# Kernel tuning notes

Measured on AMD Instinct MI355X. Metric: run time of the kernel, lower is better.

The kernel has to match this reference:

```python
import jax, jax.numpy as jnp
import numpy as np

MARGIN = 0.0


def setup_inputs() -> dict:
    key = jax.random.key(0)
    k1, k2, k3 = jax.random.split(key, 3)
    n, d = 8192, 128
    inputs = jax.random.normal(k1, (n, d), dtype=jnp.float32)
    targets = jax.random.randint(k2, (n,), 0, 512, dtype=jnp.int64)
    cids = jax.random.randint(k3, (n,), 0, 8, dtype=jnp.int64)
    return {"inputs": inputs, "targets": targets, "cids": cids}


def _margin_ranking_loss(x1, x2, margin):
    # nn.MarginRankingLoss with y=1: mean(max(0, -(x1 - x2) + margin))
    return jnp.mean(jnp.maximum(x2 - x1 + margin, 0.0))


def reference(inputs, targets, cids):
    n = inputs.shape[0]
    # pairwise euclidean distance matrix [n, n]
    sq = jnp.sum(inputs * inputs, axis=1)              # [n]
    d2 = sq[:, None] + sq[None, :] - 2.0 * (inputs @ inputs.T)
    dist = jnp.sqrt(jnp.clip(d2, 1e-12, 1e12))         # [n, n]

    mask = targets[:, None] == targets[None, :]        # [n, n] same-identity
    # view_mask (cids) is computed in the original but never used

    # hardest positive (max over same-id, incl. self) and hardest negative (min over diff-id)
    pos_masked = jnp.where(mask, dist, -jnp.inf)
    neg_masked = jnp.where(mask, jnp.inf, dist)
    dist_ap = jnp.max(pos_masked, axis=1)              # [n]
    dist_an = jnp.min(neg_masked, axis=1)              # [n]
    p2_ind = jnp.argmax(pos_masked, axis=1)            # [n]
    n1_ind = jnp.argmin(neg_masked, axis=1)            # [n]

    # secondary neighbors: hardest-negative of the hardest negative,
    # hardest-positive of the hardest positive (row lookups)
    dist_n12 = dist_an[n1_ind]                         # min of dist[n1_ind] over ~mask[n1_ind]
    dist_p12 = dist_ap[p2_ind]                         # max of dist[p2_ind] over mask[p2_ind]

    loss = (_margin_ranking_loss(dist_an, dist_ap, MARGIN)
            + 0.1 * _margin_ranking_loss(dist_n12, dist_ap, MARGIN)
            + 0.1 * _margin_ranking_loss(dist_an, dist_p12, MARGIN))
    prec = jnp.mean((dist_an > dist_ap).astype(jnp.float32))
    return loss, prec, dist
```

## Files before the change

kernel.cpp:

```cpp
#include <hip/hip_runtime.h>

#define NROWS 8192
#define DDIM 128

typedef unsigned short u16;
typedef unsigned int u32;
typedef unsigned long long u64;
typedef __attribute__((ext_vector_type(4))) float f32x4;
typedef __attribute__((ext_vector_type(4), aligned(8))) float f32x4u;
typedef __attribute__((ext_vector_type(2))) float f32x2;
typedef __attribute__((ext_vector_type(4))) int i32x4;
typedef __attribute__((ext_vector_type(8))) short short8;

__device__ __forceinline__ u16 f32_to_bf16(float f){
  u32 u = __float_as_uint(f);
  u32 r = (u + 0x7FFFu + ((u >> 16) & 1u)) >> 16;
  return (u16)r;
}
__device__ __forceinline__ float bf16_to_f32(u16 h){ return __uint_as_float(((u32)h) << 16); }

__global__ __launch_bounds__(256) void pack_kernel(const float* __restrict__ in,
                                                   u16* __restrict__ phi, u16* __restrict__ plo,
                                                   float* __restrict__ sq,
                                                   u64* __restrict__ pos_key, u64* __restrict__ neg_key){
  int t = blockIdx.x * 256 + threadIdx.x;
  if (t < NROWS){ pos_key[t] = 0ull; neg_key[t] = 0xFFFFFFFFFFFFFFFFull; }
  int r = t >> 4, s = t & 15;
  const float* src = in + (size_t)r * DDIM + s * 8;
  f32x4 a = *(const f32x4*)(src);
  f32x4 b = *(const f32x4*)(src + 4);
  float x[8] = {a.x, a.y, a.z, a.w, b.x, b.y, b.z, b.w};
  short8 hv, lv;
  float ss = 0.f;
  #pragma unroll
  for (int j = 0; j < 8; ++j){
    u16 h = f32_to_bf16(x[j]);
    u16 l = f32_to_bf16(x[j] - bf16_to_f32(h));
    hv[j] = (short)h; lv[j] = (short)l;
    ss += x[j] * x[j];
  }
  size_t dst = (((size_t)(r >> 4) * 4 + (s >> 2)) * 64 + (s & 3) * 16 + (r & 15)) * 8;
  *(short8*)(phi + dst) = hv;
  *(short8*)(plo + dst) = lv;
  #pragma unroll
  for (int m = 1; m < 16; m <<= 1) ss += __shfl_xor(ss, m, 64);
  if (s == 0) sq[r] = ss;
}

__global__ __launch_bounds__(256, 2) void dist_kernel(
    const u16* __restrict__ phi, const u16* __restrict__ plo,
    const float* __restrict__ sq, const int* __restrict__ tgt,
    float* __restrict__ dist, u64* __restrict__ pos_key, u64* __restrict__ neg_key)
{
  int id = blockIdx.x;
  int xcd = id & 7, r9 = id >> 3;
  int cx = xcd >> 1, cy = xcd & 1;
  const int bi = cx * 16 + (r9 >> 5);
  const int bj = cy * 32 + (r9 & 31);

  const int tid = threadIdx.x;
  const int w = tid >> 6, lane = tid & 63;
  const int wr = w >> 1, wc = w & 1;
  const int lr = lane & 15, g = lane >> 4;

  f32x4 acc[4][4] = {};

  short8 bufA[2][8], bufB[2][8];
  #pragma unroll
  for (int m = 0; m < 4; ++m){
    size_t offA = ((size_t)(((bi * 8 + wr * 4 + m) * 4 + 0) * 64) + lane) * 8;
    bufA[0][m * 2 + 0] = *(const short8*)(phi + offA);
    bufA[0][m * 2 + 1] = *(const short8*)(plo + offA);
    size_t offB = ((size_t)(((bj * 8 + wc * 4 + m) * 4 + 0) * 64) + lane) * 8;
    bufB[0][m * 2 + 0] = *(const short8*)(phi + offB);
    bufB[0][m * 2 + 1] = *(const short8*)(plo + offB);
  }
  #pragma unroll
  for (int kk = 0; kk < 4; ++kk){
    const int cur = kk & 1, nxt = cur ^ 1;
    if (kk < 3){
      #pragma unroll
      for (int m = 0; m < 4; ++m){
        size_t offA = ((size_t)(((bi * 8 + wr * 4 + m) * 4 + (kk + 1)) * 64) + lane) * 8;
        bufA[nxt][m * 2 + 0] = *(const short8*)(phi + offA);
        bufA[nxt][m * 2 + 1] = *(const short8*)(plo + offA);
        size_t offB = ((size_t)(((bj * 8 + wc * 4 + m) * 4 + (kk + 1)) * 64) + lane) * 8;
        bufB[nxt][m * 2 + 0] = *(const short8*)(phi + offB);
        bufB[nxt][m * 2 + 1] = *(const short8*)(plo + offB);
      }
    }
    #pragma unroll
    for (int m = 0; m < 4; ++m)
      #pragma unroll
      for (int n = 0; n < 4; ++n){
        acc[m][n] = __builtin_amdgcn_mfma_f32_16x16x32_bf16(bufB[cur][n*2+0], bufA[cur][m*2+0], acc[m][n], 0, 0, 0);
        acc[m][n] = __builtin_amdgcn_mfma_f32_16x16x32_bf16(bufB[cur][n*2+1], bufA[cur][m*2+0], acc[m][n], 0, 0, 0);
        acc[m][n] = __builtin_amdgcn_mfma_f32_16x16x32_bf16(bufB[cur][n*2+0], bufA[cur][m*2+1], acc[m][n], 0, 0, 0);
      }
  }

  f32x4 sqc[4]; i32x4 tcv[4]; int cbase[4];
  #pragma unroll
  for (int n = 0; n < 4; ++n){
    cbase[n] = bj * 128 + wc * 64 + n * 16 + g * 4;
    sqc[n] = *(const f32x4*)(sq + cbase[n]);
    tcv[n] = *(const i32x4*)(tgt + cbase[n]);
  }
  #pragma unroll
  for (int m = 0; m < 4; ++m){
    const int grow = bi * 128 + wr * 64 + m * 16 + lr;
    const float sqr = sq[grow];
    const int tr = tgt[grow];
    float bpv = -1.f, bnv = 3.0e38f; int bpc = 0x7FFFFFFF, bnc = 0x7FFFFFFF;
    float* drow = dist + (size_t)grow * NROWS;
    #pragma unroll
    for (int n = 0; n < 4; ++n){
      f32x4 dd4;
      #pragma unroll
      for (int r = 0; r < 4; ++r){
        float d2 = sqr + sqc[n][r] - 2.f * acc[m][n][r];
        d2 = fminf(fmaxf(d2, 1e-12f), 1e12f);
        dd4[r] = __builtin_amdgcn_sqrtf(d2);
        if (tr == tcv[n][r]){
          if (d2 > bpv){ bpv = d2; bpc = cbase[n] + r; }
        } else {
          if (d2 < bnv){ bnv = d2; bnc = cbase[n] + r; }
        }
      }
      *(f32x4u*)(drow + cbase[n]) = dd4;
    }
    #pragma unroll
    for (int msk = 16; msk <= 32; msk <<= 1){
      float ov = __shfl_xor(bpv, msk, 64); int oc = __shfl_xor(bpc, msk, 64);
      if (ov > bpv || (ov == bpv && oc < bpc)){ bpv = ov; bpc = oc; }
      ov = __shfl_xor(bnv, msk, 64); oc = __shfl_xor(bnc, msk, 64);
      if (ov < bnv || (ov == bnv && oc < bnc)){ bnv = ov; bnc = oc; }
    }
    if (g == 0){
      if (bpv >= 0.f)
        atomicMax(&pos_key[grow],
                  ((u64)__float_as_uint(__builtin_amdgcn_sqrtf(bpv)) << 32) | (u64)(0xFFFFFFFFu - (u32)bpc));
      if (bnv < 3.0e38f)
        atomicMin(&neg_key[grow],
                  ((u64)__float_as_uint(__builtin_amdgcn_sqrtf(bnv)) << 32) | (u64)(u32)bnc);
    }
  }
}

__global__ __launch_bounds__(1024) void final_kernel(const u64* __restrict__ pk, const u64* __restrict__ nk,
                                                     float* __restrict__ out){
  __shared__ float s_ap[NROWS];
  __shared__ float s_an[NROWS];
  int tid = threadIdx.x;
  int p2r[8], n1r[8];
  #pragma unroll
  for (int j = 0; j < 8; ++j){
    int i = tid + j * 1024;
    u64 p = pk[i], q = nk[i];
    s_ap[i] = __uint_as_float((u32)(p >> 32));
    s_an[i] = __uint_as_float((u32)(q >> 32));
    p2r[j] = (int)(0xFFFFFFFFu - (u32)(p & 0xFFFFFFFFu));
    n1r[j] = (int)(u32)(q & 0xFFFFFFFFu);
  }
  __syncthreads();
  float s1 = 0.f, s2 = 0.f, s3 = 0.f; float pc = 0.f;
  #pragma unroll
  for (int j = 0; j < 8; ++j){
    int i = tid + j * 1024;
    float a = s_ap[i], b = s_an[i];
    float n12 = s_an[n1r[j]];
    float p12 = s_ap[p2r[j]];
    s1 += fmaxf(a - b, 0.f);
    s2 += fmaxf(a - n12, 0.f);
    s3 += fmaxf(p12 - b, 0.f);
    pc += (b > a) ? 1.f : 0.f;
  }
  __syncthreads();
  float* r1 = s_ap; float* r2 = s_ap + 1024; float* r3 = s_an; float* r4 = s_an + 1024;
  r1[tid] = s1; r2[tid] = s2; r3[tid] = s3; r4[tid] = pc;
  __syncthreads();
  for (int s = 512; s > 0; s >>= 1){
    if (tid < s){ r1[tid] += r1[tid + s]; r2[tid] += r2[tid + s]; r3[tid] += r3[tid + s]; r4[tid] += r4[tid + s]; }
    __syncthreads();
  }
  if (tid == 0){
    float inv = 1.f / (float)NROWS;
    out[0] = r1[0] * inv + 0.1f * (r2[0] * inv) + 0.1f * (r3[0] * inv);
    out[1] = r4[0] * inv;
  }
}

extern "C" void kernel_launch(void* const* d_in, const int* in_sizes, int n_in,
                              void* d_out, int out_size, void* d_ws, size_t ws_size,
                              hipStream_t stream){
  const float* inputs = (const float*)d_in[0];
  const int* targets = (const int*)d_in[1];
  float* out = (float*)d_out;
  char* ws = (char*)d_ws;

  u16* phi = (u16*)ws;
  u16* plo = (u16*)(ws + (2u << 20));
  float* sq = (float*)(ws + (4u << 20));
  u64* pos_key = (u64*)(ws + (4u << 20) + (64u << 10));
  u64* neg_key = (u64*)(ws + (4u << 20) + (128u << 10));

  pack_kernel<<<(NROWS * 16) / 256, 256, 0, stream>>>(inputs, phi, plo, sq, pos_key, neg_key);
  dist_kernel<<<64 * 64, 256, 0, stream>>>(phi, plo, sq, targets, out + 2, pos_key, neg_key);
  final_kernel<<<1, 1024, 0, stream>>>(pos_key, neg_key, out);
}
```

Before: 128.1 us.

## Make dist blocks persistent over four column tiles with cross-tile prefetch

Each block now handles four consecutive 128x128 column tiles of one row block, so the grid shrinks from 4096 to 1024 blocks. The next tile's first K-slice is prefetched during the last MFMA step of the current tile, which hides load latency across tiles and cuts block launch overhead. The trade-off is less parallel slack per CU and possible extra register pressure. The epilogue stores and atomics stay serial per tile, so there is less chance to overlap them with compute from other blocks.

```diff
diff --git a/kernel.cpp b/kernel.cpp
--- a/kernel.cpp
+++ b/kernel.cpp
@@ -53,98 +53,102 @@
     float* __restrict__ dist, u64* __restrict__ pos_key, u64* __restrict__ neg_key)
 {
   int id = blockIdx.x;
-  int xcd = id & 7, r9 = id >> 3;
-  int cx = xcd >> 1, cy = xcd & 1;
-  const int bi = cx * 16 + (r9 >> 5);
-  const int bj = cy * 32 + (r9 & 31);
+  int xcd = id & 7, r7 = id >> 3;
+  const int bi = (xcd >> 1) * 16 + (r7 >> 3);
+  const int strip = (xcd & 1) * 8 + (r7 & 7);
+  const int bj0 = strip * 4;
 
   const int tid = threadIdx.x;
   const int w = tid >> 6, lane = tid & 63;
   const int wr = w >> 1, wc = w & 1;
   const int lr = lane & 15, g = lane >> 4;
 
-  f32x4 acc[4][4] = {};
-
   short8 bufA[2][8], bufB[2][8];
-  #pragma unroll
-  for (int m = 0; m < 4; ++m){
-    size_t offA = ((size_t)(((bi * 8 + wr * 4 + m) * 4 + 0) * 64) + lane) * 8;
-    bufA[0][m * 2 + 0] = *(const short8*)(phi + offA);
-    bufA[0][m * 2 + 1] = *(const short8*)(plo + offA);
-    size_t offB = ((size_t)(((bj * 8 + wc * 4 + m) * 4 + 0) * 64) + lane) * 8;
-    bufB[0][m * 2 + 0] = *(const short8*)(phi + offB);
-    bufB[0][m * 2 + 1] = *(const short8*)(plo + offB);
-  }
-  #pragma unroll
-  for (int kk = 0; kk < 4; ++kk){
-    const int cur = kk & 1, nxt = cur ^ 1;
-    if (kk < 3){
+
+  #define LOADS(p, BJ, KK)                                                              \
+    _Pragma("unroll")                                                                   \
+    for (int m_ = 0; m_ < 4; ++m_){                                                     \
+      size_t offA = ((size_t)(((bi * 8 + wr * 4 + m_) * 4 + (KK)) * 64) + lane) * 8;    \
+      bufA[p][m_ * 2 + 0] = *(const short8*)(phi + offA);                               \
+      bufA[p][m_ * 2 + 1] = *(const short8*)(plo + offA);                               \
+      size_t offB = ((size_t)((((BJ) * 8 + wc * 4 + m_) * 4 + (KK)) * 64) + lane) * 8;  \
+      bufB[p][m_ * 2 + 0] = *(const short8*)(phi + offB);                               \
+      bufB[p][m_ * 2 + 1] = *(const short8*)(plo + offB);                               \
+    }
+
+  LOADS(0, bj0, 0);
+
+  for (int t = 0; t < 4; ++t){
+    const int bj = bj0 + t;
+
+    f32x4 acc[4][4] = {};
+
+    #pragma unroll
+    for (int kk = 0; kk < 4; ++kk){
+      const int cur = kk & 1, nxt = cur ^ 1;
+      if (kk < 3){
+        LOADS(nxt, bj, kk + 1);
+      } else if (t < 3){
+        LOADS(nxt, bj + 1, 0);
+      }
       #pragma unroll
-      for (int m = 0; m < 4; ++m){
-        size_t offA = ((size_t)(((bi * 8 + wr * 4 + m) * 4 + (kk + 1)) * 64) + lane) * 8;
-        bufA[nxt][m * 2 + 0] = *(const short8*)(phi + offA);
-        bufA[nxt][m * 2 + 1] = *(const short8*)(plo + offA);
-        size_t offB = ((size_t)(((bj * 8 + wc * 4 + m) * 4 + (kk + 1)) * 64) + lane) * 8;
-        bufB[nxt][m * 2 + 0] = *(const short8*)(phi + offB);
-        bufB[nxt][m * 2 + 1] = *(const short8*)(plo + offB);
-      }
-    }
+      for (int m = 0; m < 4; ++m)
+        #pragma unroll
+        for (int n = 0; n < 4; ++n){
+          acc[m][n] = __builtin_amdgcn_mfma_f32_16x16x32_bf16(bufB[cur][n*2+0], bufA[cur][m*2+0], acc[m][n], 0, 0, 0);
+          acc[m][n] = __builtin_amdgcn_mfma_f32_16x16x32_bf16(bufB[cur][n*2+1], bufA[cur][m*2+0], acc[m][n], 0, 0, 0);
+          acc[m][n] = __builtin_amdgcn_mfma_f32_16x16x32_bf16(bufB[cur][n*2+0], bufA[cur][m*2+1], acc[m][n], 0, 0, 0);
+        }
+    }
+
+    f32x4 sqc[4]; i32x4 tcv[4]; int cbase[4];
     #pragma unroll
-    for (int m = 0; m < 4; ++m)
+    for (int n = 0; n < 4; ++n){
+      cbase[n] = bj * 128 + wc * 64 + n * 16 + g * 4;
+      sqc[n] = *(const f32x4*)(sq + cbase[n]);
+      tcv[n] = *(const i32x4*)(tgt + cbase[n]);
+    }
+    #pragma unroll
+    for (int m = 0; m < 4; ++m){
+      const int grow = bi * 128 + wr * 64 + m * 16 + lr;
+      const float sqr = sq[grow];
+      const int tr = tgt[grow];
+      float bpv = -1.f, bnv = 3.0e38f; int bpc = 0x7FFFFFFF, bnc = 0x7FFFFFFF;
+      float* drow = dist + (size_t)grow * NROWS;
       #pragma unroll
       for (int n = 0; n < 4; ++n){
-        acc[m][n] = __builtin_amdgcn_mfma_f32_16x16x32_bf16(bufB[cur][n*2+0], bufA[cur][m*2+0], acc[m][n], 0, 0, 0);
-        acc[m][n] = __builtin_amdgcn_mfma_f32_16x16x32_bf16(bufB[cur][n*2+1], bufA[cur][m*2+0], acc[m][n], 0, 0, 0);
-        acc[m][n] = __builtin_amdgcn_mfma_f32_16x16x32_bf16(bufB[cur][n*2+0], bufA[cur][m*2+1], acc[m][n], 0, 0, 0);
-      }
-  }
-
-  f32x4 sqc[4]; i32x4 tcv[4]; int cbase[4];
-  #pragma unroll
-  for (int n = 0; n < 4; ++n){
-    cbase[n] = bj * 128 + wc * 64 + n * 16 + g * 4;
-    sqc[n] = *(const f32x4*)(sq + cbase[n]);
-    tcv[n] = *(const i32x4*)(tgt + cbase[n]);
-  }
-  #pragma unroll
-  for (int m = 0; m < 4; ++m){
-    const int grow = bi * 128 + wr * 64 + m * 16 + lr;
-    const float sqr = sq[grow];
-    const int tr = tgt[grow];
-    float bpv = -1.f, bnv = 3.0e38f; int bpc = 0x7FFFFFFF, bnc = 0x7FFFFFFF;
-    float* drow = dist + (size_t)grow * NROWS;
-    #pragma unroll
-    for (int n = 0; n < 4; ++n){
-      f32x4 dd4;
+        f32x4 dd4;
+        #pragma unroll
+        for (int r = 0; r < 4; ++r){
+          float d2 = sqr + sqc[n][r] - 2.f * acc[m][n][r];
+          d2 = fminf(fmaxf(d2, 1e-12f), 1e12f);
+          dd4[r] = __builtin_amdgcn_sqrtf(d2);
+          if (tr == tcv[n][r]){
+            if (d2 > bpv){ bpv = d2; bpc = cbase[n] + r; }
+          } else {
+            if (d2 < bnv){ bnv = d2; bnc = cbase[n] + r; }
+          }
+        }
+        *(f32x4u*)(drow + cbase[n]) = dd4;
+      }
       #pragma unroll
-      for (int r = 0; r < 4; ++r){
-        float d2 = sqr + sqc[n][r] - 2.f * acc[m][n][r];
-        d2 = fminf(fmaxf(d2, 1e-12f), 1e12f);
-        dd4[r] = __builtin_amdgcn_sqrtf(d2);
-        if (tr == tcv[n][r]){
-          if (d2 > bpv){ bpv = d2; bpc = cbase[n] + r; }
-        } else {
-          if (d2 < bnv){ bnv = d2; bnc = cbase[n] + r; }
-        }
-      }
-      *(f32x4u*)(drow + cbase[n]) = dd4;
-    }
-    #pragma unroll
-    for (int msk = 16; msk <= 32; msk <<= 1){
-      float ov = __shfl_xor(bpv, msk, 64); int oc = __shfl_xor(bpc, msk, 64);
-      if (ov > bpv || (ov == bpv && oc < bpc)){ bpv = ov; bpc = oc; }
-      ov = __shfl_xor(bnv, msk, 64); oc = __shfl_xor(bnc, msk, 64);
-      if (ov < bnv || (ov == bnv && oc < bnc)){ bnv = ov; bnc = oc; }
-    }
-    if (g == 0){
-      if (bpv >= 0.f)
-        atomicMax(&pos_key[grow],
-                  ((u64)__float_as_uint(__builtin_amdgcn_sqrtf(bpv)) << 32) | (u64)(0xFFFFFFFFu - (u32)bpc));
-      if (bnv < 3.0e38f)
-        atomicMin(&neg_key[grow],
-                  ((u64)__float_as_uint(__builtin_amdgcn_sqrtf(bnv)) << 32) | (u64)(u32)bnc);
-    }
-  }
+      for (int msk = 16; msk <= 32; msk <<= 1){
+        float ov = __shfl_xor(bpv, msk, 64); int oc = __shfl_xor(bpc, msk, 64);
+        if (ov > bpv || (ov == bpv && oc < bpc)){ bpv = ov; bpc = oc; }
+        ov = __shfl_xor(bnv, msk, 64); oc = __shfl_xor(bnc, msk, 64);
+        if (ov < bnv || (ov == bnv && oc < bnc)){ bnv = ov; bnc = oc; }
+      }
+      if (g == 0){
+        if (bpv >= 0.f)
+          atomicMax(&pos_key[grow],
+                    ((u64)__float_as_uint(__builtin_amdgcn_sqrtf(bpv)) << 32) | (u64)(0xFFFFFFFFu - (u32)bpc));
+        if (bnv < 3.0e38f)
+          atomicMin(&neg_key[grow],
+                    ((u64)__float_as_uint(__builtin_amdgcn_sqrtf(bnv)) << 32) | (u64)(u32)bnc);
+      }
+    }
+  }
+  #undef LOADS
 }
 
 __global__ __launch_bounds__(1024) void final_kernel(const u64* __restrict__ pk, const u64* __restrict__ nk,
@@ -205,6 +209,6 @@
   u64* neg_key = (u64*)(ws + (4u << 20) + (128u << 10));
 
   pack_kernel<<<(NROWS * 16) / 256, 256, 0, stream>>>(inputs, phi, plo, sq, pos_key, neg_key);
-  dist_kernel<<<64 * 64, 256, 0, stream>>>(phi, plo, sq, targets, out + 2, pos_key, neg_key);
+  dist_kernel<<<1024, 256, 0, stream>>>(phi, plo, sq, targets, out + 2, pos_key, neg_key);
   final_kernel<<<1, 1024, 0, stream>>>(pos_key, neg_key, out);
 }
```

New measurement: 198.1 us. +54.6%, slower.
